# Kernel tuning notes

Measured on AMD Instinct MI355X. Metric: run time of the kernel, lower is better.

The kernel has to match this reference:

```python
import jax, jax.numpy as jnp
import numpy as np

CLASS_NUM = 31
KERNEL_MUL = 2.0
KERNEL_NUM = 5


def setup_inputs() -> dict:
    key = jax.random.key(0)
    k1, k2, k3, k4 = jax.random.split(key, 4)
    source = jax.random.normal(k1, (2048, 2048), dtype=jnp.float32)
    target = jax.random.normal(k2, (2048, 2048), dtype=jnp.float32)
    s_label = jax.random.randint(k3, (2048,), 0, CLASS_NUM)
    t_label = jax.random.normal(k4, (2048, CLASS_NUM), dtype=jnp.float32)
    return {"source": source, "target": target, "s_label": s_label, "t_label": t_label}


def _mmd_loss(source, target, s_label, t_label):
    ns = source.shape[0]
    nt = target.shape[0]
    t_hard = jnp.argmax(t_label, axis=1)                       # hard target labels
    labels = jnp.concatenate([s_label, t_hard], axis=0)        # [N]
    total = jnp.concatenate([source, target], axis=0)          # [N, D]
    # pairwise squared euclidean distances via gram trick (same math as
    # ((x_i - x_j)**2).sum(-1), fused instead of the NxNxD expansion)
    sq = jnp.sum(total * total, axis=-1)                       # [N]
    D2 = sq[:, None] + sq[None, :] - 2.0 * (total @ total.T)   # [N, N]
    sign = jnp.concatenate([jnp.ones((ns,), D2.dtype), -jnp.ones((nt,), D2.dtype)])
    sign_pair = sign[:, None] * sign[None, :]                  # [N, N] (+SS,+TT,-ST,-TS)
    is_src = jnp.concatenate([jnp.ones((ns,), D2.dtype), jnp.zeros((nt,), D2.dtype)])
    bw_scale = KERNEL_MUL ** (KERNEL_NUM // 2)

    def per_class(carry, c):
        loss_acc, cnt = carry
        m = (labels == c).astype(D2.dtype)                     # [N]
        n_src = jnp.sum(m * is_src)
        n_tgt = jnp.sum(m * (1.0 - is_src))
        present = (n_src > 0) & (n_tgt > 0)                    # class in both domains
        n = n_src + n_tgt
        pair = m[:, None] * m[None, :]                         # [N, N] class mask
        # bandwidth from detached (.data) within-class distances
        l2sum = jax.lax.stop_gradient(jnp.sum(D2 * pair))
        denom = jnp.maximum(n * n - n, 1.0)
        bw = (l2sum / denom) / bw_scale
        bw = jnp.where(present, jnp.maximum(bw, 1e-20), 1.0)   # safe when absent
        K = jnp.zeros_like(D2)
        for i in range(KERNEL_NUM):
            K = K + jnp.exp(-D2 / (bw * (KERNEL_MUL ** i)))
        contrib = jnp.sum(pair * sign_pair * K) / jnp.maximum(n * n, 1.0)
        loss_acc = loss_acc + jnp.where(present, contrib, 0.0)
        cnt = cnt + jnp.where(present, 1.0, 0.0)
        return (loss_acc, cnt), None

    (loss, cnt), _ = jax.lax.scan(per_class, (jnp.float32(0.0), jnp.float32(0.0)),
                                  jnp.arange(CLASS_NUM))
    return loss / cnt


def reference(source, target, s_label, t_label):
    return _mmd_loss(source, target, s_label, t_label)
```

## Files before the change

### kernel.cpp

```cpp
#include <hip/hip_runtime.h>

typedef __attribute__((ext_vector_type(8))) short bf16x8;
typedef __attribute__((ext_vector_type(4))) float f32x4;

#define TILE 32

__device__ __forceinline__ unsigned int f2bf(float x) {
    unsigned int u = __float_as_uint(x);
    return (u + 0x7fffu + ((u >> 16) & 1u)) >> 16;
}

__global__ void k_prep(const int* __restrict__ slab, const float* __restrict__ tlab,
                       int ns, int N, int C,
                       int* __restrict__ clsrows, int* __restrict__ cnt_src,
                       int* __restrict__ fill) {
    int i = blockIdx.x * 256 + threadIdx.x;
    if (i >= N) return;
    int lab;
    if (i < ns) {
        lab = slab[i];
    } else {
        const float* row = tlab + (size_t)(i - ns) * C;
        float best = row[0];
        lab = 0;
        for (int c = 1; c < C; c++) {
            float v = row[c];
            if (v > best) { best = v; lab = c; }
        }
    }
    if (i < ns) atomicAdd(&cnt_src[lab], 1);
    int pos = atomicAdd(&fill[lab], 1);
    clsrows[(size_t)lab * N + pos] = i;
}

__global__ void k_offsets(const int* __restrict__ cnt_src, const int* __restrict__ fill,
                          int C,
                          int* __restrict__ rowOff, int* __restrict__ jobOff,
                          int* __restrict__ tilesC, int* __restrict__ present,
                          double* __restrict__ inv_n2, int* __restrict__ nJobsP) {
    int lane = threadIdx.x;
    int n = (lane < C) ? fill[lane] : 0;
    int nsrc = (lane < C) ? cnt_src[lane] : 0;
    int pres = (nsrc > 0 && (n - nsrc) > 0) ? 1 : 0;
    int T = pres ? (n + TILE - 1) / TILE : 0;
    int jobs = T * T;
    int sn = n, sj = jobs;
    for (int o = 1; o < 64; o <<= 1) {
        int vn = __shfl_up(sn, o);
        int vj = __shfl_up(sj, o);
        if (lane >= o) { sn += vn; sj += vj; }
    }
    if (lane < C) {
        rowOff[lane] = sn - n;
        jobOff[lane] = sj - jobs;
        tilesC[lane] = T;
        present[lane] = pres;
        double nn = (double)n * (double)n;
        if (nn < 1.0) nn = 1.0;
        inv_n2[lane] = 1.0 / nn;
    }
    if (lane == C - 1) { rowOff[C] = sn; jobOff[C] = sj; *nJobsP = sj; }
}

__global__ __launch_bounds__(256) void k_gather(
        const float* __restrict__ src, const float* __restrict__ tgt,
        const int* __restrict__ clsrows, const int* __restrict__ rowOff,
        int ns, int N, int D, int C,
        unsigned short* __restrict__ Xg, float* __restrict__ sqg, float* __restrict__ sgg) {
    int s = blockIdx.x;
    int tid = threadIdx.x;
    __shared__ int ro[64];
    if (tid <= C) ro[tid] = rowOff[tid];
    __syncthreads();
    int c = 0;
    while (c + 1 <= C && ro[c + 1] <= s) c++;
    int g = clsrows[(size_t)c * N + (s - ro[c])];
    const float* row = (g < ns) ? src + (size_t)g * D : tgt + (size_t)(g - ns) * D;
    unsigned int* orow = (unsigned int*)(Xg + (size_t)s * D);
    float acc = 0.f;
    int iters = D / 512;
    for (int it = 0; it < iters; it++) {
        float2 v = *(const float2*)(row + it * 512 + tid * 2);
        acc += v.x * v.x + v.y * v.y;
        orow[it * 256 + tid] = f2bf(v.x) | (f2bf(v.y) << 16);
    }
    for (int o = 32; o; o >>= 1) acc += __shfl_down(acc, o);
    __shared__ float ls[4];
    if ((tid & 63) == 0) ls[tid >> 6] = acc;
    __syncthreads();
    if (tid == 0) {
        sqg[s] = ls[0] + ls[1] + ls[2] + ls[3];
        sgg[s] = (g < ns) ? 1.f : -1.f;
    }
}

__global__ void k_classum(const unsigned short* __restrict__ Xg,
                          const int* __restrict__ rowOff, int D,
                          float* __restrict__ classum) {
    int c = blockIdx.x;
    int chunk = blockIdx.y;
    int split = blockIdx.z;
    int b = rowOff[c], e = rowOff[c + 1];
    int n = e - b;
    int per = (n + 3) / 4;
    int r0 = split * per, r1 = min(n, r0 + per);
    int d = chunk * 512 + threadIdx.x * 2;
    float a0 = 0.f, a1 = 0.f;
    for (int r = r0; r < r1; r++) {
        unsigned int u = *(const unsigned int*)(Xg + (size_t)(b + r) * D + d);
        a0 += __uint_as_float(u << 16);
        a1 += __uint_as_float(u & 0xffff0000u);
    }
    if (r1 > r0) {
        atomicAdd(&classum[(size_t)c * D + d], a0);
        atomicAdd(&classum[(size_t)c * D + d + 1], a1);
    }
}

__global__ void k_bwC(const float* __restrict__ sqg, const float* __restrict__ classum,
                      const int* __restrict__ rowOff, const int* __restrict__ present,
                      int D, float* __restrict__ invbw) {
    int c = blockIdx.x;
    int lane = threadIdx.x;
    int b = rowOff[c], e = rowOff[c + 1];
    int n = e - b;
    double sq = 0.0;
    for (int i = b + lane; i < e; i += 64) sq += (double)sqg[i];
    double snorm = 0.0;
    const float* cs = classum + (size_t)c * D;
    for (int d = lane; d < D; d += 64) { double v = (double)cs[d]; snorm += v * v; }
    for (int o = 32; o; o >>= 1) {
        sq += __shfl_down(sq, o);
        snorm += __shfl_down(snorm, o);
    }
    if (lane == 0) {
        double l2sum = 2.0 * (double)n * sq - 2.0 * snorm;
        double denom = (double)n * (double)n - (double)n;
        if (denom < 1.0) denom = 1.0;
        double bw = l2sum / denom / 4.0;
        bw = present[c] ? fmax(bw, 1e-20) : 1.0;
        double m = 1.0;
        for (int k = 0; k < 5; k++) { invbw[c * 8 + k] = (float)(1.0 / (bw * m)); m *= 2.0; }
    }
}

__global__ __launch_bounds__(64) void k_pairs(
        const unsigned short* __restrict__ Xg, const float* __restrict__ sqg,
        const float* __restrict__ sgg, const float* __restrict__ invbw,
        const int* __restrict__ jobOff, const int* __restrict__ tilesC,
        const int* __restrict__ rowOff, const int* __restrict__ nJobsP,
        int D, int C, double* __restrict__ contrib) {
    int lane = threadIdx.x;
    int nJobs = *nJobsP;
    int jo = (lane <= C) ? jobOff[lane] : 0x7fffffff;

    for (int job = blockIdx.x; job < nJobs; job += gridDim.x) {
        unsigned long long m = __ballot(jo <= job);
        int c = __popcll(m) - 1;
        int jobbase = __shfl(jo, c);
        int T = tilesC[c];
        int t = job - jobbase;
        int ti = t / T, tj = t - ti * T;
        int base = rowOff[c];
        int n = rowOff[c + 1] - base;

        int kgrp = lane >> 4;
        int lr = lane & 15;
        int riA0 = min(ti * TILE + lr, n - 1);
        int riA1 = min(ti * TILE + lr + 16, n - 1);
        int riB0 = min(tj * TILE + lr, n - 1);
        int riB1 = min(tj * TILE + lr + 16, n - 1);
        const unsigned short* pA0 = Xg + (size_t)(base + riA0) * D + kgrp * 8;
        const unsigned short* pA1 = Xg + (size_t)(base + riA1) * D + kgrp * 8;
        const unsigned short* pB0 = Xg + (size_t)(base + riB0) * D + kgrp * 8;
        const unsigned short* pB1 = Xg + (size_t)(base + riB1) * D + kgrp * 8;

        f32x4 acc[2][2];
        acc[0][0] = (f32x4){0.f, 0.f, 0.f, 0.f};
        acc[0][1] = acc[0][0]; acc[1][0] = acc[0][0]; acc[1][1] = acc[0][0];

        #pragma unroll 4
        for (int k0 = 0; k0 < D; k0 += 32) {
            bf16x8 a0 = *(const bf16x8*)(pA0 + k0);
            bf16x8 a1 = *(const bf16x8*)(pA1 + k0);
            bf16x8 b0 = *(const bf16x8*)(pB0 + k0);
            bf16x8 b1 = *(const bf16x8*)(pB1 + k0);
            acc[0][0] = __builtin_amdgcn_mfma_f32_16x16x32_bf16(a0, b0, acc[0][0], 0, 0, 0);
            acc[0][1] = __builtin_amdgcn_mfma_f32_16x16x32_bf16(a0, b1, acc[0][1], 0, 0, 0);
            acc[1][0] = __builtin_amdgcn_mfma_f32_16x16x32_bf16(a1, b0, acc[1][0], 0, 0, 0);
            acc[1][1] = __builtin_amdgcn_mfma_f32_16x16x32_bf16(a1, b1, acc[1][1], 0, 0, 0);
        }

        float ib0 = invbw[c * 8 + 0], ib1 = invbw[c * 8 + 1], ib2 = invbw[c * 8 + 2];
        float ib3 = invbw[c * 8 + 3], ib4 = invbw[c * 8 + 4];

        int crow = (lane >> 4) * 4;
        float tsum = 0.f;
        #pragma unroll
        for (int fj = 0; fj < 2; fj++) {
            int lj = fj * 16 + lr + tj * TILE;
            bool vj = lj < n;
            int cj = base + (vj ? lj - tj * TILE + tj * TILE : 0);
            cj = base + (vj ? lj : 0);
            float sB = sqg[cj];
            float gB = sgg[cj];
            #pragma unroll
            for (int fi = 0; fi < 2; fi++) {
                #pragma unroll
                for (int r = 0; r < 4; r++) {
                    int li = fi * 16 + crow + r + ti * TILE;
                    bool vi = li < n;
                    int ci = base + (vi ? li : 0);
                    float sA = sqg[ci];
                    float gA = sgg[ci];
                    float a = acc[fi][fj][r];
                    float D2 = sA + sB - 2.f * a;
                    float e = expf(-D2 * ib0) + expf(-D2 * ib1) + expf(-D2 * ib2)
                            + expf(-D2 * ib3) + expf(-D2 * ib4);
                    tsum += (vi && vj) ? gA * gB * e : 0.f;
                }
            }
        }
        double dsum = (double)tsum;
        for (int o = 32; o; o >>= 1) dsum += __shfl_down(dsum, o);
        if (lane == 0) atomicAdd(&contrib[c], dsum);
    }
}

__global__ void k_final(const double* __restrict__ contrib, const int* __restrict__ present,
                        const double* __restrict__ inv_n2, int C, float* __restrict__ out) {
    int c = threadIdx.x;
    double l = 0.0, k = 0.0;
    if (c < C && present[c]) { l = contrib[c] * inv_n2[c]; k = 1.0; }
    for (int o = 32; o; o >>= 1) { l += __shfl_down(l, o); k += __shfl_down(k, o); }
    if (c == 0) out[0] = (float)(l / k);
}

extern "C" void kernel_launch(void* const* d_in, const int* in_sizes, int n_in,
                              void* d_out, int out_size, void* d_ws, size_t ws_size,
                              hipStream_t stream) {
    const float* src  = (const float*)d_in[0];
    const float* tgt  = (const float*)d_in[1];
    const int*   slab = (const int*)d_in[2];
    const float* tlab = (const float*)d_in[3];
    const int ns = in_sizes[2];
    const int D  = in_sizes[0] / ns;
    const int nt = in_sizes[1] / D;
    const int C  = in_sizes[3] / nt;
    const int N  = ns + nt;

    char* w = (char*)d_ws;
    size_t off = 0;
    auto take = [&](size_t bytes) -> char* {
        char* p = w + off;
        off = (off + bytes + 255) & ~(size_t)255;
        return p;
    };
    int*    cnt_src = (int*)take(C * sizeof(int));
    int*    fill    = (int*)take(C * sizeof(int));
    double* contrib = (double*)take(C * sizeof(double));
    float*  classum = (float*)take((size_t)C * D * sizeof(float));
    size_t zbytes = off;
    int*    clsrows = (int*)take((size_t)C * N * sizeof(int));
    int*    rowOff  = (int*)take((C + 1) * sizeof(int));
    int*    jobOff  = (int*)take((C + 1) * sizeof(int));
    int*    tilesC  = (int*)take(C * sizeof(int));
    int*    present = (int*)take(C * sizeof(int));
    double* inv_n2  = (double*)take(C * sizeof(double));
    float*  invbw   = (float*)take((size_t)C * 8 * sizeof(float));
    int*    nJobsP  = (int*)take(sizeof(int));
    unsigned short* Xg = (unsigned short*)take((size_t)N * D * sizeof(unsigned short));
    float*  sqg     = (float*)take((size_t)N * sizeof(float));
    float*  sgg     = (float*)take((size_t)N * sizeof(float));
    (void)ws_size; (void)n_in; (void)out_size;

    hipMemsetAsync(d_ws, 0, zbytes, stream);
    k_prep<<<(N + 255) / 256, 256, 0, stream>>>(slab, tlab, ns, N, C, clsrows, cnt_src, fill);
    k_offsets<<<1, 64, 0, stream>>>(cnt_src, fill, C, rowOff, jobOff, tilesC, present,
                                    inv_n2, nJobsP);
    k_gather<<<N, 256, 0, stream>>>(src, tgt, clsrows, rowOff, ns, N, D, C, Xg, sqg, sgg);
    dim3 gcs(C, D / 512, 4);
    k_classum<<<gcs, 256, 0, stream>>>(Xg, rowOff, D, classum);
    k_bwC<<<C, 64, 0, stream>>>(sqg, classum, rowOff, present, D, invbw);
    k_pairs<<<1024, 64, 0, stream>>>(Xg, sqg, sgg, invbw, jobOff, tilesC, rowOff,
                                     nJobsP, D, C, contrib);
    k_final<<<1, 64, 0, stream>>>(contrib, present, inv_n2, C, (float*)d_out);
}
```

Before: 152.8 us.

## Fuse all stages into one persistent kernel with grid barriers and split-K Gram reuse

Replaces the seven-kernel pipeline with a single persistent kernel of 512 blocks that uses atomic grid barriers between stages: labeling, per-class offsets, gather/bf16 conversion, Gram tile computation, bandwidth, kernel-sum and final reduction. The within-class L2 sum is now taken from the Gram tiles directly, replacing the class-sum pass. The first Gram pass is split four ways along K to raise parallelism, and its partial tiles are saved to workspace so the exp pass can reload them instead of recomputing the matmul. This removes launch overhead and the duplicate matmul, but depends on all 512 blocks being co-resident for the spin barriers and adds workspace traffic for the partial tiles.

```diff
diff --git a/kernel.cpp b/kernel.cpp
--- a/kernel.cpp
+++ b/kernel.cpp
@@ -3,237 +3,269 @@
 typedef __attribute__((ext_vector_type(8))) short bf16x8;
 typedef __attribute__((ext_vector_type(4))) float f32x4;
 
-#define TILE 32
-
-__device__ __forceinline__ unsigned int f2bf(float x) {
-    unsigned int u = __float_as_uint(x);
+#define NBLK 512
+#define NTHR 512
+#define NWAVES (NBLK * 8)
+
+__device__ __forceinline__ unsigned f2bf(float x) {
+    unsigned u = __float_as_uint(x);
     return (u + 0x7fffu + ((u >> 16) & 1u)) >> 16;
 }
 
-__global__ void k_prep(const int* __restrict__ slab, const float* __restrict__ tlab,
-                       int ns, int N, int C,
-                       int* __restrict__ clsrows, int* __restrict__ cnt_src,
-                       int* __restrict__ fill) {
-    int i = blockIdx.x * 256 + threadIdx.x;
-    if (i >= N) return;
-    int lab;
-    if (i < ns) {
-        lab = slab[i];
-    } else {
-        const float* row = tlab + (size_t)(i - ns) * C;
-        float best = row[0];
-        lab = 0;
-        for (int c = 1; c < C; c++) {
-            float v = row[c];
-            if (v > best) { best = v; lab = c; }
-        }
-    }
-    if (i < ns) atomicAdd(&cnt_src[lab], 1);
-    int pos = atomicAdd(&fill[lab], 1);
-    clsrows[(size_t)lab * N + pos] = i;
+__device__ __forceinline__ void gbar(unsigned* bar) {
+    __syncthreads();
+    if (threadIdx.x == 0) {
+        __threadfence();
+        atomicAdd(bar, 1u);
+        while (__hip_atomic_load(bar, __ATOMIC_ACQUIRE, __HIP_MEMORY_SCOPE_AGENT) < NBLK)
+            __builtin_amdgcn_s_sleep(1);
+        __threadfence();
+    }
+    __syncthreads();
 }
 
-__global__ void k_offsets(const int* __restrict__ cnt_src, const int* __restrict__ fill,
-                          int C,
-                          int* __restrict__ rowOff, int* __restrict__ jobOff,
-                          int* __restrict__ tilesC, int* __restrict__ present,
-                          double* __restrict__ inv_n2, int* __restrict__ nJobsP) {
-    int lane = threadIdx.x;
-    int n = (lane < C) ? fill[lane] : 0;
-    int nsrc = (lane < C) ? cnt_src[lane] : 0;
-    int pres = (nsrc > 0 && (n - nsrc) > 0) ? 1 : 0;
-    int T = pres ? (n + TILE - 1) / TILE : 0;
-    int jobs = T * T;
-    int sn = n, sj = jobs;
-    for (int o = 1; o < 64; o <<= 1) {
-        int vn = __shfl_up(sn, o);
-        int vj = __shfl_up(sj, o);
-        if (lane >= o) { sn += vn; sj += vj; }
-    }
-    if (lane < C) {
-        rowOff[lane] = sn - n;
-        jobOff[lane] = sj - jobs;
-        tilesC[lane] = T;
-        present[lane] = pres;
-        double nn = (double)n * (double)n;
-        if (nn < 1.0) nn = 1.0;
-        inv_n2[lane] = 1.0 / nn;
-    }
-    if (lane == C - 1) { rowOff[C] = sn; jobOff[C] = sj; *nJobsP = sj; }
-}
-
-__global__ __launch_bounds__(256) void k_gather(
+__global__ __launch_bounds__(NTHR, 4) void k_all(
         const float* __restrict__ src, const float* __restrict__ tgt,
-        const int* __restrict__ clsrows, const int* __restrict__ rowOff,
+        const int* __restrict__ slab, const float* __restrict__ tlab,
         int ns, int N, int D, int C,
-        unsigned short* __restrict__ Xg, float* __restrict__ sqg, float* __restrict__ sgg) {
-    int s = blockIdx.x;
-    int tid = threadIdx.x;
-    __shared__ int ro[64];
-    if (tid <= C) ro[tid] = rowOff[tid];
+        int* __restrict__ clsrows, int* __restrict__ cnt_src, int* __restrict__ fill,
+        unsigned* __restrict__ bars, double* __restrict__ gramsum,
+        double* __restrict__ contrib,
+        unsigned short* __restrict__ Xg, float* __restrict__ sqg, float* __restrict__ sgg,
+        float* __restrict__ Pbuf, int capTiles, float* __restrict__ out) {
+    const int tid = threadIdx.x;
+    const int lane = tid & 63;
+    const int w = tid >> 6;
+    const int b = blockIdx.x;
+
+    __shared__ int roS[33], tpoS[33], tS[32], presS[32];
+    __shared__ float invbwS[32 * 5];
+    __shared__ double inv_n2S[32];
+    __shared__ int nTilesS;
+
+    for (int i = b * 8 + w; i < N; i += NWAVES) {
+        int lab;
+        if (i < ns) {
+            lab = slab[i];
+        } else {
+            float v = -3.4e38f; int idx = C;
+            if (lane < C) { v = tlab[(size_t)(i - ns) * C + lane]; idx = lane; }
+            for (int o = 32; o; o >>= 1) {
+                float v2 = __shfl_xor(v, o);
+                int i2 = __shfl_xor(idx, o);
+                if (v2 > v || (v2 == v && i2 < idx)) { v = v2; idx = i2; }
+            }
+            lab = idx;
+        }
+        if (lane == 0) {
+            if (i < ns) atomicAdd(&cnt_src[lab], 1);
+            int pos = atomicAdd(&fill[lab], 1);
+            clsrows[(size_t)lab * N + pos] = i;
+        }
+    }
+    gbar(bars + 0);
+
+    if (w == 0) {
+        int n = (lane < C) ? fill[lane] : 0;
+        int nsrc = (lane < C) ? cnt_src[lane] : 0;
+        int pres = (nsrc > 0 && (n - nsrc) > 0) ? 1 : 0;
+        int T = pres ? (n + 31) / 32 : 0;
+        int t2 = T * T;
+        int sn = n, sp = t2;
+        for (int o = 1; o < 64; o <<= 1) {
+            int a = __shfl_up(sn, o), c2 = __shfl_up(sp, o);
+            if (lane >= o) { sn += a; sp += c2; }
+        }
+        if (lane < C) {
+            roS[lane] = sn - n; tpoS[lane] = sp - t2;
+            tS[lane] = T; presS[lane] = pres;
+            double nn = (double)n * (double)n; if (nn < 1.0) nn = 1.0;
+            inv_n2S[lane] = 1.0 / nn;
+        }
+        if (lane == C - 1) { roS[C] = sn; tpoS[C] = sp; nTilesS = sp; }
+    }
     __syncthreads();
-    int c = 0;
-    while (c + 1 <= C && ro[c + 1] <= s) c++;
-    int g = clsrows[(size_t)c * N + (s - ro[c])];
-    const float* row = (g < ns) ? src + (size_t)g * D : tgt + (size_t)(g - ns) * D;
-    unsigned int* orow = (unsigned int*)(Xg + (size_t)s * D);
-    float acc = 0.f;
-    int iters = D / 512;
-    for (int it = 0; it < iters; it++) {
-        float2 v = *(const float2*)(row + it * 512 + tid * 2);
-        acc += v.x * v.x + v.y * v.y;
-        orow[it * 256 + tid] = f2bf(v.x) | (f2bf(v.y) << 16);
-    }
-    for (int o = 32; o; o >>= 1) acc += __shfl_down(acc, o);
-    __shared__ float ls[4];
-    if ((tid & 63) == 0) ls[tid >> 6] = acc;
+
+    for (int s = b * 8 + w; s < N; s += NWAVES) {
+        int c = __popcll(__ballot((lane < C) && (roS[lane] <= s))) - 1;
+        int g = clsrows[(size_t)c * N + (s - roS[c])];
+        const float* row = (g < ns) ? src + (size_t)g * D : tgt + (size_t)(g - ns) * D;
+        unsigned short* orow = Xg + (size_t)s * D;
+        float acc = 0.f;
+        for (int it = 0; it < D / 256; ++it) {
+            float4 v = *(const float4*)(row + it * 256 + lane * 4);
+            acc += v.x * v.x + v.y * v.y + v.z * v.z + v.w * v.w;
+            uint2 p;
+            p.x = f2bf(v.x) | (f2bf(v.y) << 16);
+            p.y = f2bf(v.z) | (f2bf(v.w) << 16);
+            *(uint2*)(orow + it * 256 + lane * 4) = p;
+        }
+        for (int o = 32; o; o >>= 1) acc += __shfl_down(acc, o);
+        if (lane == 0) { sqg[s] = acc; sgg[s] = (g < ns) ? 1.f : -1.f; }
+    }
+    gbar(bars + 1);
+
+    {
+        int nTiles = nTilesS;
+        int nJobsK = nTiles * 4;
+        int KC = D / 4;
+        int kgrp = lane >> 4, lr = lane & 15, crow = (lane >> 4) * 4;
+        for (int j = b * 8 + w; j < nJobsK; j += NWAVES) {
+            int kc = j / nTiles;
+            int tile = j - kc * nTiles;
+            int c = __popcll(__ballot((lane < C) && (tpoS[lane] <= tile))) - 1;
+            int t = tile - tpoS[c];
+            int T = tS[c];
+            int ti = t / T, tj = t - ti * T;
+            int base = roS[c];
+            int n = roS[c + 1] - base;
+
+            int riA0 = min(ti * 32 + lr, n - 1), riA1 = min(ti * 32 + lr + 16, n - 1);
+            int riB0 = min(tj * 32 + lr, n - 1), riB1 = min(tj * 32 + lr + 16, n - 1);
+            const unsigned short* pA0 = Xg + (size_t)(base + riA0) * D + kc * KC + kgrp * 8;
+            const unsigned short* pA1 = Xg + (size_t)(base + riA1) * D + kc * KC + kgrp * 8;
+            const unsigned short* pB0 = Xg + (size_t)(base + riB0) * D + kc * KC + kgrp * 8;
+            const unsigned short* pB1 = Xg + (size_t)(base + riB1) * D + kc * KC + kgrp * 8;
+
+            f32x4 a00 = (f32x4){0.f, 0.f, 0.f, 0.f}, a01 = a00, a10 = a00, a11 = a00;
+            #pragma unroll 4
+            for (int k0 = 0; k0 < KC; k0 += 32) {
+                bf16x8 va0 = *(const bf16x8*)(pA0 + k0);
+                bf16x8 va1 = *(const bf16x8*)(pA1 + k0);
+                bf16x8 vb0 = *(const bf16x8*)(pB0 + k0);
+                bf16x8 vb1 = *(const bf16x8*)(pB1 + k0);
+                a00 = __builtin_amdgcn_mfma_f32_16x16x32_bf16(va0, vb0, a00, 0, 0, 0);
+                a01 = __builtin_amdgcn_mfma_f32_16x16x32_bf16(va0, vb1, a01, 0, 0, 0);
+                a10 = __builtin_amdgcn_mfma_f32_16x16x32_bf16(va1, vb0, a10, 0, 0, 0);
+                a11 = __builtin_amdgcn_mfma_f32_16x16x32_bf16(va1, vb1, a11, 0, 0, 0);
+            }
+
+            float gsum = 0.f;
+            float* Pb = Pbuf + ((size_t)tile * 4 + kc) * 1024 + lane * 4;
+            bool store = (tile < capTiles);
+            if (store) *(f32x4*)(Pb + 0 * 256) = a00;
+            if (store) *(f32x4*)(Pb + 1 * 256) = a01;
+            if (store) *(f32x4*)(Pb + 2 * 256) = a10;
+            if (store) *(f32x4*)(Pb + 3 * 256) = a11;
+            #pragma unroll
+            for (int r = 0; r < 4; r++) {
+                int li0 = ti * 32 + crow + r, li1 = li0 + 16;
+                int lj0 = tj * 32 + lr,       lj1 = lj0 + 16;
+                if (li0 < n && lj0 < n) gsum += a00[r];
+                if (li0 < n && lj1 < n) gsum += a01[r];
+                if (li1 < n && lj0 < n) gsum += a10[r];
+                if (li1 < n && lj1 < n) gsum += a11[r];
+            }
+            double gs = (double)gsum;
+            for (int o = 32; o; o >>= 1) gs += __shfl_down(gs, o);
+            if (lane == 0) atomicAdd(&gramsum[c], gs);
+        }
+    }
+    gbar(bars + 2);
+
+    for (int c = w; c < C; c += 8) {
+        int bs = roS[c], en = roS[c + 1], n = en - bs;
+        double s = 0.0;
+        for (int i = bs + lane; i < en; i += 64) s += (double)sqg[i];
+        for (int o = 32; o; o >>= 1) s += __shfl_down(s, o);
+        if (lane == 0) {
+            double l2 = 2.0 * (double)n * s - 2.0 * gramsum[c];
+            double den = (double)n * (double)n - (double)n; if (den < 1.0) den = 1.0;
+            double bw = l2 / den / 4.0;
+            bw = presS[c] ? fmax(bw, 1e-20) : 1.0;
+            double m = 1.0;
+            for (int k = 0; k < 5; k++) { invbwS[c * 5 + k] = (float)(1.0 / (bw * m)); m *= 2.0; }
+        }
+    }
     __syncthreads();
-    if (tid == 0) {
-        sqg[s] = ls[0] + ls[1] + ls[2] + ls[3];
-        sgg[s] = (g < ns) ? 1.f : -1.f;
-    }
-}
-
-__global__ void k_classum(const unsigned short* __restrict__ Xg,
-                          const int* __restrict__ rowOff, int D,
-                          float* __restrict__ classum) {
-    int c = blockIdx.x;
-    int chunk = blockIdx.y;
-    int split = blockIdx.z;
-    int b = rowOff[c], e = rowOff[c + 1];
-    int n = e - b;
-    int per = (n + 3) / 4;
-    int r0 = split * per, r1 = min(n, r0 + per);
-    int d = chunk * 512 + threadIdx.x * 2;
-    float a0 = 0.f, a1 = 0.f;
-    for (int r = r0; r < r1; r++) {
-        unsigned int u = *(const unsigned int*)(Xg + (size_t)(b + r) * D + d);
-        a0 += __uint_as_float(u << 16);
-        a1 += __uint_as_float(u & 0xffff0000u);
-    }
-    if (r1 > r0) {
-        atomicAdd(&classum[(size_t)c * D + d], a0);
-        atomicAdd(&classum[(size_t)c * D + d + 1], a1);
-    }
-}
-
-__global__ void k_bwC(const float* __restrict__ sqg, const float* __restrict__ classum,
-                      const int* __restrict__ rowOff, const int* __restrict__ present,
-                      int D, float* __restrict__ invbw) {
-    int c = blockIdx.x;
-    int lane = threadIdx.x;
-    int b = rowOff[c], e = rowOff[c + 1];
-    int n = e - b;
-    double sq = 0.0;
-    for (int i = b + lane; i < e; i += 64) sq += (double)sqg[i];
-    double snorm = 0.0;
-    const float* cs = classum + (size_t)c * D;
-    for (int d = lane; d < D; d += 64) { double v = (double)cs[d]; snorm += v * v; }
-    for (int o = 32; o; o >>= 1) {
-        sq += __shfl_down(sq, o);
-        snorm += __shfl_down(snorm, o);
-    }
-    if (lane == 0) {
-        double l2sum = 2.0 * (double)n * sq - 2.0 * snorm;
-        double denom = (double)n * (double)n - (double)n;
-        if (denom < 1.0) denom = 1.0;
-        double bw = l2sum / denom / 4.0;
-        bw = present[c] ? fmax(bw, 1e-20) : 1.0;
-        double m = 1.0;
-        for (int k = 0; k < 5; k++) { invbw[c * 8 + k] = (float)(1.0 / (bw * m)); m *= 2.0; }
-    }
-}
-
-__global__ __launch_bounds__(64) void k_pairs(
-        const unsigned short* __restrict__ Xg, const float* __restrict__ sqg,
-        const float* __restrict__ sgg, const float* __restrict__ invbw,
-        const int* __restrict__ jobOff, const int* __restrict__ tilesC,
-        const int* __restrict__ rowOff, const int* __restrict__ nJobsP,
-        int D, int C, double* __restrict__ contrib) {
-    int lane = threadIdx.x;
-    int nJobs = *nJobsP;
-    int jo = (lane <= C) ? jobOff[lane] : 0x7fffffff;
-
-    for (int job = blockIdx.x; job < nJobs; job += gridDim.x) {
-        unsigned long long m = __ballot(jo <= job);
-        int c = __popcll(m) - 1;
-        int jobbase = __shfl(jo, c);
-        int T = tilesC[c];
-        int t = job - jobbase;
-        int ti = t / T, tj = t - ti * T;
-        int base = rowOff[c];
-        int n = rowOff[c + 1] - base;
-
-        int kgrp = lane >> 4;
-        int lr = lane & 15;
-        int riA0 = min(ti * TILE + lr, n - 1);
-        int riA1 = min(ti * TILE + lr + 16, n - 1);
-        int riB0 = min(tj * TILE + lr, n - 1);
-        int riB1 = min(tj * TILE + lr + 16, n - 1);
-        const unsigned short* pA0 = Xg + (size_t)(base + riA0) * D + kgrp * 8;
-        const unsigned short* pA1 = Xg + (size_t)(base + riA1) * D + kgrp * 8;
-        const unsigned short* pB0 = Xg + (size_t)(base + riB0) * D + kgrp * 8;
-        const unsigned short* pB1 = Xg + (size_t)(base + riB1) * D + kgrp * 8;
-
-        f32x4 acc[2][2];
-        acc[0][0] = (f32x4){0.f, 0.f, 0.f, 0.f};
-        acc[0][1] = acc[0][0]; acc[1][0] = acc[0][0]; acc[1][1] = acc[0][0];
-
-        #pragma unroll 4
-        for (int k0 = 0; k0 < D; k0 += 32) {
-            bf16x8 a0 = *(const bf16x8*)(pA0 + k0);
-            bf16x8 a1 = *(const bf16x8*)(pA1 + k0);
-            bf16x8 b0 = *(const bf16x8*)(pB0 + k0);
-            bf16x8 b1 = *(const bf16x8*)(pB1 + k0);
-            acc[0][0] = __builtin_amdgcn_mfma_f32_16x16x32_bf16(a0, b0, acc[0][0], 0, 0, 0);
-            acc[0][1] = __builtin_amdgcn_mfma_f32_16x16x32_bf16(a0, b1, acc[0][1], 0, 0, 0);
-            acc[1][0] = __builtin_amdgcn_mfma_f32_16x16x32_bf16(a1, b0, acc[1][0], 0, 0, 0);
-            acc[1][1] = __builtin_amdgcn_mfma_f32_16x16x32_bf16(a1, b1, acc[1][1], 0, 0, 0);
-        }
-
-        float ib0 = invbw[c * 8 + 0], ib1 = invbw[c * 8 + 1], ib2 = invbw[c * 8 + 2];
-        float ib3 = invbw[c * 8 + 3], ib4 = invbw[c * 8 + 4];
-
-        int crow = (lane >> 4) * 4;
-        float tsum = 0.f;
-        #pragma unroll
-        for (int fj = 0; fj < 2; fj++) {
-            int lj = fj * 16 + lr + tj * TILE;
-            bool vj = lj < n;
-            int cj = base + (vj ? lj - tj * TILE + tj * TILE : 0);
-            cj = base + (vj ? lj : 0);
-            float sB = sqg[cj];
-            float gB = sgg[cj];
+
+    {
+        int nTiles = nTilesS;
+        int kgrp = lane >> 4, lr = lane & 15, crow = (lane >> 4) * 4;
+        for (int tile = b * 8 + w; tile < nTiles; tile += NWAVES) {
+            int c = __popcll(__ballot((lane < C) && (tpoS[lane] <= tile))) - 1;
+            int t = tile - tpoS[c];
+            int T = tS[c];
+            int ti = t / T, tj = t - ti * T;
+            int base = roS[c];
+            int n = roS[c + 1] - base;
+
+            f32x4 a00, a01, a10, a11;
+            if (tile < capTiles) {
+                const float* Pb = Pbuf + (size_t)tile * 4096 + lane * 4;
+                a00 = (f32x4){0.f, 0.f, 0.f, 0.f}; a01 = a00; a10 = a00; a11 = a00;
+                #pragma unroll
+                for (int kc = 0; kc < 4; kc++) {
+                    a00 += *(const f32x4*)(Pb + kc * 1024 + 0 * 256);
+                    a01 += *(const f32x4*)(Pb + kc * 1024 + 1 * 256);
+                    a10 += *(const f32x4*)(Pb + kc * 1024 + 2 * 256);
+                    a11 += *(const f32x4*)(Pb + kc * 1024 + 3 * 256);
+                }
+            } else {
+                int riA0 = min(ti * 32 + lr, n - 1), riA1 = min(ti * 32 + lr + 16, n - 1);
+                int riB0 = min(tj * 32 + lr, n - 1), riB1 = min(tj * 32 + lr + 16, n - 1);
+                const unsigned short* pA0 = Xg + (size_t)(base + riA0) * D + kgrp * 8;
+                const unsigned short* pA1 = Xg + (size_t)(base + riA1) * D + kgrp * 8;
+                const unsigned short* pB0 = Xg + (size_t)(base + riB0) * D + kgrp * 8;
+                const unsigned short* pB1 = Xg + (size_t)(base + riB1) * D + kgrp * 8;
+                a00 = (f32x4){0.f, 0.f, 0.f, 0.f}; a01 = a00; a10 = a00; a11 = a00;
+                for (int k0 = 0; k0 < D; k0 += 32) {
+                    bf16x8 va0 = *(const bf16x8*)(pA0 + k0);
+                    bf16x8 va1 = *(const bf16x8*)(pA1 + k0);
+                    bf16x8 vb0 = *(const bf16x8*)(pB0 + k0);
+                    bf16x8 vb1 = *(const bf16x8*)(pB1 + k0);
+                    a00 = __builtin_amdgcn_mfma_f32_16x16x32_bf16(va0, vb0, a00, 0, 0, 0);
+                    a01 = __builtin_amdgcn_mfma_f32_16x16x32_bf16(va0, vb1, a01, 0, 0, 0);
+                    a10 = __builtin_amdgcn_mfma_f32_16x16x32_bf16(va1, vb0, a10, 0, 0, 0);
+                    a11 = __builtin_amdgcn_mfma_f32_16x16x32_bf16(va1, vb1, a11, 0, 0, 0);
+                }
+            }
+
+            float ib0 = invbwS[c * 5 + 0], ib1 = invbwS[c * 5 + 1], ib2 = invbwS[c * 5 + 2];
+            float ib3 = invbwS[c * 5 + 3], ib4 = invbwS[c * 5 + 4];
+            int lj0 = tj * 32 + lr, lj1 = lj0 + 16;
+            float sB0 = sqg[base + min(lj0, n - 1)], gB0 = sgg[base + min(lj0, n - 1)];
+            float sB1 = sqg[base + min(lj1, n - 1)], gB1 = sgg[base + min(lj1, n - 1)];
+            float tsum = 0.f;
             #pragma unroll
-            for (int fi = 0; fi < 2; fi++) {
-                #pragma unroll
-                for (int r = 0; r < 4; r++) {
-                    int li = fi * 16 + crow + r + ti * TILE;
-                    bool vi = li < n;
-                    int ci = base + (vi ? li : 0);
-                    float sA = sqg[ci];
-                    float gA = sgg[ci];
-                    float a = acc[fi][fj][r];
-                    float D2 = sA + sB - 2.f * a;
-                    float e = expf(-D2 * ib0) + expf(-D2 * ib1) + expf(-D2 * ib2)
-                            + expf(-D2 * ib3) + expf(-D2 * ib4);
-                    tsum += (vi && vj) ? gA * gB * e : 0.f;
-                }
-            }
-        }
-        double dsum = (double)tsum;
-        for (int o = 32; o; o >>= 1) dsum += __shfl_down(dsum, o);
-        if (lane == 0) atomicAdd(&contrib[c], dsum);
-    }
-}
-
-__global__ void k_final(const double* __restrict__ contrib, const int* __restrict__ present,
-                        const double* __restrict__ inv_n2, int C, float* __restrict__ out) {
-    int c = threadIdx.x;
-    double l = 0.0, k = 0.0;
-    if (c < C && present[c]) { l = contrib[c] * inv_n2[c]; k = 1.0; }
-    for (int o = 32; o; o >>= 1) { l += __shfl_down(l, o); k += __shfl_down(k, o); }
-    if (c == 0) out[0] = (float)(l / k);
+            for (int r = 0; r < 4; r++) {
+                int li0 = ti * 32 + crow + r, li1 = li0 + 16;
+                float sA0 = sqg[base + min(li0, n - 1)], gA0 = sgg[base + min(li0, n - 1)];
+                float sA1 = sqg[base + min(li1, n - 1)], gA1 = sgg[base + min(li1, n - 1)];
+                if (li0 < n && lj0 < n) {
+                    float D2 = sA0 + sB0 - 2.f * a00[r];
+                    tsum += gA0 * gB0 * (expf(-D2 * ib0) + expf(-D2 * ib1) + expf(-D2 * ib2)
+                                       + expf(-D2 * ib3) + expf(-D2 * ib4));
+                }
+                if (li0 < n && lj1 < n) {
+                    float D2 = sA0 + sB1 - 2.f * a01[r];
+                    tsum += gA0 * gB1 * (expf(-D2 * ib0) + expf(-D2 * ib1) + expf(-D2 * ib2)
+                                       + expf(-D2 * ib3) + expf(-D2 * ib4));
+                }
+                if (li1 < n && lj0 < n) {
+                    float D2 = sA1 + sB0 - 2.f * a10[r];
+                    tsum += gA1 * gB0 * (expf(-D2 * ib0) + expf(-D2 * ib1) + expf(-D2 * ib2)
+                                       + expf(-D2 * ib3) + expf(-D2 * ib4));
+                }
+                if (li1 < n && lj1 < n) {
+                    float D2 = sA1 + sB1 - 2.f * a11[r];
+                    tsum += gA1 * gB1 * (expf(-D2 * ib0) + expf(-D2 * ib1) + expf(-D2 * ib2)
+                                       + expf(-D2 * ib3) + expf(-D2 * ib4));
+                }
+            }
+            double ds = (double)tsum;
+            for (int o = 32; o; o >>= 1) ds += __shfl_down(ds, o);
+            if (lane == 0) atomicAdd(&contrib[c], ds);
+        }
+    }
+    gbar(bars + 3);
+
+    if (b == 0 && w == 0) {
+        double l = 0.0, k = 0.0;
+        if (lane < C && presS[lane]) { l = contrib[lane] * inv_n2S[lane]; k = 1.0; }
+        for (int o = 32; o; o >>= 1) { l += __shfl_down(l, o); k += __shfl_down(k, o); }
+        if (lane == 0) out[0] = (float)(l / k);
+    }
 }
 
 extern "C" void kernel_launch(void* const* d_in, const int* in_sizes, int n_in,
@@ -256,33 +288,24 @@
         off = (off + bytes + 255) & ~(size_t)255;
         return p;
     };
-    int*    cnt_src = (int*)take(C * sizeof(int));
-    int*    fill    = (int*)take(C * sizeof(int));
-    double* contrib = (double*)take(C * sizeof(double));
-    float*  classum = (float*)take((size_t)C * D * sizeof(float));
+    int*      cnt_src = (int*)take(32 * sizeof(int));
+    int*      fill    = (int*)take(32 * sizeof(int));
+    unsigned* bars    = (unsigned*)take(8 * sizeof(unsigned));
+    double*   gramsum = (double*)take(32 * sizeof(double));
+    double*   contrib = (double*)take(32 * sizeof(double));
     size_t zbytes = off;
-    int*    clsrows = (int*)take((size_t)C * N * sizeof(int));
-    int*    rowOff  = (int*)take((C + 1) * sizeof(int));
-    int*    jobOff  = (int*)take((C + 1) * sizeof(int));
-    int*    tilesC  = (int*)take(C * sizeof(int));
-    int*    present = (int*)take(C * sizeof(int));
-    double* inv_n2  = (double*)take(C * sizeof(double));
-    float*  invbw   = (float*)take((size_t)C * 8 * sizeof(float));
-    int*    nJobsP  = (int*)take(sizeof(int));
-    unsigned short* Xg = (unsigned short*)take((size_t)N * D * sizeof(unsigned short));
-    float*  sqg     = (float*)take((size_t)N * sizeof(float));
-    float*  sgg     = (float*)take((size_t)N * sizeof(float));
-    (void)ws_size; (void)n_in; (void)out_size;
+    int*            clsrows = (int*)take((size_t)C * N * sizeof(int));
+    float*          sqg     = (float*)take((size_t)N * sizeof(float));
+    float*          sgg     = (float*)take((size_t)N * sizeof(float));
+    unsigned short* Xg      = (unsigned short*)take((size_t)N * D * sizeof(unsigned short));
+    size_t remain = (ws_size > off) ? (ws_size - off) : 0;
+    long long capLL = (long long)(remain / (4096ull * sizeof(float)));
+    int capTiles = (int)((capLL > 65536) ? 65536 : capLL);
+    float* Pbuf = (float*)(w + off);
+    (void)n_in; (void)out_size;
 
     hipMemsetAsync(d_ws, 0, zbytes, stream);
-    k_prep<<<(N + 255) / 256, 256, 0, stream>>>(slab, tlab, ns, N, C, clsrows, cnt_src, fill);
-    k_offsets<<<1, 64, 0, stream>>>(cnt_src, fill, C, rowOff, jobOff, tilesC, present,
-                                    inv_n2, nJobsP);
-    k_gather<<<N, 256, 0, stream>>>(src, tgt, clsrows, rowOff, ns, N, D, C, Xg, sqg, sgg);
-    dim3 gcs(C, D / 512, 4);
-    k_classum<<<gcs, 256, 0, stream>>>(Xg, rowOff, D, classum);
-    k_bwC<<<C, 64, 0, stream>>>(sqg, classum, rowOff, present, D, invbw);
-    k_pairs<<<1024, 64, 0, stream>>>(Xg, sqg, sgg, invbw, jobOff, tilesC, rowOff,
-                                     nJobsP, D, C, contrib);
-    k_final<<<1, 64, 0, stream>>>(contrib, present, inv_n2, C, (float*)d_out);
+    k_all<<<NBLK, NTHR, 0, stream>>>(src, tgt, slab, tlab, ns, N, D, C,
+                                     clsrows, cnt_src, fill, bars, gramsum, contrib,
+                                     Xg, sqg, sgg, Pbuf, capTiles, (float*)d_out);
 }
```

After: 469.0 us. 3.07x slower.
